# Kernel tuning notes

Hardware: AMD Instinct MI355X
Metric: run time of the kernel (lower is better)

## Reference

```python
import jax, jax.numpy as jnp
import numpy as np

N_NODES = 100000
FEAT = 128
N_EDGES = 1600000


def setup_inputs() -> dict:
    key = jax.random.key(0)
    k1, k2, k3, k4, k5 = jax.random.split(key, 5)
    weight = jax.random.normal(k1, (N_NODES, FEAT), dtype=jnp.float32)
    cj = jax.random.uniform(k2, (N_NODES, 1), dtype=jnp.float32)
    ci = jax.random.uniform(k3, (N_NODES, 1), dtype=jnp.float32)
    src = jax.random.randint(k4, (N_EDGES,), 0, N_NODES, dtype=jnp.int32)
    dst = jax.random.randint(k5, (N_EDGES,), 0, N_NODES, dtype=jnp.int32)
    return {"weight": weight, "cj": cj, "ci": ci, "src": src, "dst": dst}


def reference(weight, cj, ci, src, dst):
    # feat = weight * dropout(cj); dropout_rate=0.0 -> identity
    feat = weight * cj                      # [N, F]
    msgs = feat[src]                        # [E, F] copy_src gather
    h = jax.ops.segment_sum(msgs, dst, num_segments=weight.shape[0])  # [N, F]
    return h * ci                           # dst-side normalize
```

## Files before the change

kernel.cpp:

```cpp
#include <hip/hip_runtime.h>
#include <hip/hip_bf16.h>

#define FEAT 128
#define BINW 128
#define BINSHIFT 7
#define TB 8192
#define MAXBIN 1024
#define MAXTILE 256
#define FS_CAP 4096

__device__ __forceinline__ unsigned short f2b(float f) {
    __hip_bfloat16 h = __float2bfloat16(f);
    return *reinterpret_cast<unsigned short*>(&h);
}
__device__ __forceinline__ float b2f_lo(unsigned u) {
    unsigned x = u << 16;
    float f;
    __builtin_memcpy(&f, &x, 4);
    return f;
}
__device__ __forceinline__ float b2f_hi(unsigned u) {
    unsigned x = u & 0xFFFF0000u;
    float f;
    __builtin_memcpy(&f, &x, 4);
    return f;
}
__device__ __forceinline__ unsigned int pack2(float lo, float hi) {
    return (unsigned int)f2b(lo) | ((unsigned int)f2b(hi) << 16);
}


__global__ void convert_kernel(const float* __restrict__ weight,
                               const float* __restrict__ cj,
                               unsigned short* __restrict__ feat16, int N) {
    int i = blockIdx.x * 256 + threadIdx.x;
    if (i >= N * (FEAT / 8)) return;
    int row = i >> 4;
    int seg = i & 15;
    float c = cj[row];
    const float4* p = reinterpret_cast<const float4*>(weight + (size_t)row * FEAT + seg * 8);
    float4 a = p[0], b = p[1];
    uint4 o;
    o.x = pack2(a.x * c, a.y * c);
    o.y = pack2(a.z * c, a.w * c);
    o.z = pack2(b.x * c, b.y * c);
    o.w = pack2(b.z * c, b.w * c);
    *reinterpret_cast<uint4*>(feat16 + (size_t)i * 8) = o;
}

__global__ void hist_bins_kernel(const int* __restrict__ dst, int* __restrict__ cnt,
                                 int E, int NBIN) {
    __shared__ int h[MAXBIN];
    int tile = blockIdx.x;
    for (int b = threadIdx.x; b < NBIN; b += 256) h[b] = 0;
    __syncthreads();
    int e0 = tile * TB;
    #pragma unroll 4
    for (int i = 0; i < TB / 256; ++i) {
        int e = e0 + i * 256 + threadIdx.x;
        if (e < E) atomicAdd(&h[dst[e] >> BINSHIFT], 1);
    }
    __syncthreads();
    for (int b = threadIdx.x; b < NBIN; b += 256) cnt[tile * NBIN + b] = h[b];
}

__global__ void bin_scan_kernel(const int* __restrict__ cnt, int* __restrict__ base_local,
                                int* __restrict__ binTot, int NBIN, int NTILE) {
    __shared__ int s[MAXTILE];
    int b = blockIdx.x;
    int t = threadIdx.x;
    int v = (t < NTILE) ? cnt[(size_t)t * NBIN + b] : 0;
    s[t] = v;
    __syncthreads();
    for (int off = 1; off < MAXTILE; off <<= 1) {
        int u = (t >= off) ? s[t - off] : 0;
        __syncthreads();
        s[t] += u;
        __syncthreads();
    }
    if (t < NTILE) base_local[(size_t)t * NBIN + b] = s[t] - v;
    if (t == MAXTILE - 1) binTot[b] = s[t];
}

__global__ void scan_tot_kernel(const int* __restrict__ binTot, int* __restrict__ binStart,
                                int NBIN) {
    __shared__ int s[1024];
    int t = threadIdx.x;
    int v = (t < NBIN) ? binTot[t] : 0;
    s[t] = v;
    __syncthreads();
    for (int off = 1; off < 1024; off <<= 1) {
        int u = (t >= off) ? s[t - off] : 0;
        __syncthreads();
        s[t] += u;
        __syncthreads();
    }
    if (t < NBIN) binStart[t] = s[t] - v;
    if (t == NBIN - 1) binStart[NBIN] = s[t];
}

__global__ void scatter_pairs_kernel(const int* __restrict__ src, const int* __restrict__ dst,
                                     const int* __restrict__ base_local,
                                     const int* __restrict__ binStart,
                                     unsigned* __restrict__ pair,
                                     int E, int NBIN) {
    __shared__ int base_l[MAXBIN];
    __shared__ int cur[MAXBIN];
    int tile = blockIdx.x;
    for (int b = threadIdx.x; b < NBIN; b += 256) {
        base_l[b] = binStart[b] + base_local[(size_t)tile * NBIN + b];
        cur[b] = 0;
    }
    __syncthreads();
    int e0 = tile * TB;
    #pragma unroll 4
    for (int i = 0; i < TB / 256; ++i) {
        int e = e0 + i * 256 + threadIdx.x;
        if (e < E) {
            int d = dst[e];
            int b = d >> BINSHIFT;
            int pos = atomicAdd(&cur[b], 1);
            pair[base_l[b] + pos] = (unsigned)src[e] | ((unsigned)(d & (BINW - 1)) << 17);
        }
    }
}

__global__ void fine_sort_kernel(unsigned* __restrict__ pair,
                                 unsigned* __restrict__ tmp,
                                 const int* __restrict__ binStart,
                                 int* __restrict__ offsets,
                                 int N, int E) {
    __shared__ int cnt[BINW];
    __shared__ int sbase[BINW];
    __shared__ unsigned stage[FS_CAP];
    int bin = blockIdx.x;
    int t = threadIdx.x;
    if (t < BINW) cnt[t] = 0;
    __syncthreads();
    int start = binStart[bin];
    int end   = binStart[bin + 1];
    bool lds_ok = (end - start) <= FS_CAP;

    if (lds_ok) {
        for (int k = start + t; k < end; k += 256) {
            unsigned p = pair[k];
            stage[k - start] = p;
            atomicAdd(&cnt[p >> 17], 1);
        }
    } else {
        for (int k = start + t; k < end; k += 256) {
            unsigned p = pair[k];
            tmp[k] = p;
            atomicAdd(&cnt[p >> 17], 1);
        }
    }
    __syncthreads();
    int mine = (t < BINW) ? cnt[t] : 0;
    if (t < BINW) sbase[t] = mine;
    __syncthreads();
    for (int d = 1; d < BINW; d <<= 1) {
        int v = 0;
        if (t < BINW && t >= d) v = sbase[t - d];
        __syncthreads();
        if (t < BINW) sbase[t] += v;
        __syncthreads();
    }
    if (t < BINW) {
        int excl = sbase[t] - mine;
        int node = (bin << BINSHIFT) + t;
        if (node < N) offsets[node] = start + excl;
        sbase[t] = start + excl;
        cnt[t] = 0;
    }
    if (bin == 0 && t == 0) offsets[N] = E;
    __syncthreads();
    if (lds_ok) {
        for (int k = start + t; k < end; k += 256) {
            unsigned p = stage[k - start];
            int ld = p >> 17;
            int pos = atomicAdd(&cnt[ld], 1);
            pair[sbase[ld] + pos] = p & 0x1FFFF;
        }
    } else {
        for (int k = start + t; k < end; k += 256) {
            unsigned p = tmp[k];
            int ld = p >> 17;
            int pos = atomicAdd(&cnt[ld], 1);
            pair[sbase[ld] + pos] = p & 0x1FFFF;
        }
    }
}

__global__ void gather_kernel(const unsigned short* __restrict__ feat16,
                              const float* __restrict__ ci,
                              const int* __restrict__ offsets,
                              const int* __restrict__ src_sorted,
                              float* __restrict__ out, int N) {
    int gt = blockIdx.x * blockDim.x + threadIdx.x;
    int node = gt >> 6;
    if (node >= N) return;
    int lane = gt & 63;
    int fi   = (lane & 15) << 3;
    int q    = lane >> 4;
    int start = offsets[node];
    int end   = offsets[node + 1];
    float acc[8] = {0.f, 0.f, 0.f, 0.f, 0.f, 0.f, 0.f, 0.f};
    #pragma unroll 2
    for (int k = start + q; k < end; k += 4) {
        int s = src_sorted[k];
        uint4 u = *reinterpret_cast<const uint4*>(feat16 + ((size_t)s << 7) + fi);
        acc[0] += b2f_lo(u.x); acc[1] += b2f_hi(u.x);
        acc[2] += b2f_lo(u.y); acc[3] += b2f_hi(u.y);
        acc[4] += b2f_lo(u.z); acc[5] += b2f_hi(u.z);
        acc[6] += b2f_lo(u.w); acc[7] += b2f_hi(u.w);
    }
    #pragma unroll
    for (int j = 0; j < 8; ++j) {
        acc[j] += __shfl_xor(acc[j], 16);
        acc[j] += __shfl_xor(acc[j], 32);
    }
    if (q == 0) {
        float c = ci[node];
        float4 v0 = make_float4(acc[0] * c, acc[1] * c, acc[2] * c, acc[3] * c);
        float4 v1 = make_float4(acc[4] * c, acc[5] * c, acc[6] * c, acc[7] * c);
        float* o = out + ((size_t)node << 7) + fi;
        *reinterpret_cast<float4*>(o)     = v0;
        *reinterpret_cast<float4*>(o + 4) = v1;
    }
}


__global__ void zero_ints_kernel(int* __restrict__ p, int n) {
    int i = blockIdx.x * blockDim.x + threadIdx.x;
    if (i < n) p[i] = 0;
}

__global__ void convert_hist_kernel(const float* __restrict__ weight,
                                    const float* __restrict__ cj,
                                    const int* __restrict__ dst,
                                    int* __restrict__ counts,
                                    unsigned short* __restrict__ feat16,
                                    int N, int E) {
    int i = blockIdx.x * blockDim.x + threadIdx.x;
    int NC = N * (FEAT / 8);
    if (i < NC) {
        int row = i >> 4;
        int seg = i & 15;
        float c = cj[row];
        const float4* p = reinterpret_cast<const float4*>(weight + (size_t)row * FEAT + seg * 8);
        float4 a = p[0], b = p[1];
        uint4 o;
        o.x = pack2(a.x * c, a.y * c);
        o.y = pack2(a.z * c, a.w * c);
        o.z = pack2(b.x * c, b.y * c);
        o.w = pack2(b.z * c, b.w * c);
        *reinterpret_cast<uint4*>(feat16 + (size_t)i * 8) = o;
    }
    if (i < E) atomicAdd(&counts[dst[i]], 1);
}

__global__ void block_sum_kernel(const int* __restrict__ counts, int* __restrict__ bsum, int N) {
    __shared__ int s[256];
    int i = blockIdx.x * 256 + threadIdx.x;
    s[threadIdx.x] = (i < N) ? counts[i] : 0;
    __syncthreads();
    for (int off = 128; off > 0; off >>= 1) {
        if (threadIdx.x < off) s[threadIdx.x] += s[threadIdx.x + off];
        __syncthreads();
    }
    if (threadIdx.x == 0) bsum[blockIdx.x] = s[0];
}

__global__ void scan_bsum_kernel(int* __restrict__ bsum, int nb) {
    __shared__ int s[512];
    int t = threadIdx.x;
    int mine = (t < nb) ? bsum[t] : 0;
    s[t] = mine;
    __syncthreads();
    for (int off = 1; off < 512; off <<= 1) {
        int v = (t >= off) ? s[t - off] : 0;
        __syncthreads();
        s[t] += v;
        __syncthreads();
    }
    if (t < nb) bsum[t] = s[t] - mine;
}

__global__ void scan_counts_kernel(const int* __restrict__ counts, const int* __restrict__ bsum,
                                   int* __restrict__ offsets, int* __restrict__ cursor,
                                   int N, int E) {
    __shared__ int s[256];
    int t = threadIdx.x;
    int i = blockIdx.x * 256 + t;
    int mine = (i < N) ? counts[i] : 0;
    s[t] = mine;
    __syncthreads();
    for (int off = 1; off < 256; off <<= 1) {
        int v = (t >= off) ? s[t - off] : 0;
        __syncthreads();
        s[t] += v;
        __syncthreads();
    }
    if (i < N) {
        int o = bsum[blockIdx.x] + s[t] - mine;
        offsets[i] = o;
        cursor[i] = o;
    }
    if (i == 0 && blockIdx.x == 0) offsets[N] = E;
}

__global__ void bucket_kernel(const int* __restrict__ src, const int* __restrict__ dst,
                              int* __restrict__ cursor,
                              int* __restrict__ src_sorted, int E) {
    int i = blockIdx.x * blockDim.x + threadIdx.x;
    if (i < E) {
        int pos = atomicAdd(&cursor[dst[i]], 1);
        src_sorted[pos] = src[i];
    }
}


__global__ void gcmc_zero_kernel(float4* __restrict__ out, int n4) {
    int i = blockIdx.x * blockDim.x + threadIdx.x;
    if (i < n4) out[i] = make_float4(0.f, 0.f, 0.f, 0.f);
}

__global__ void gcmc_scatter_kernel(const float* __restrict__ weight,
                                    const float* __restrict__ cj,
                                    const int* __restrict__ src,
                                    const int* __restrict__ dst,
                                    float* __restrict__ out,
                                    int n_edges) {
    int t = blockIdx.x * blockDim.x + threadIdx.x;
    int e = t >> 5;
    int f = (t & 31) << 2;
    if (e >= n_edges) return;
    int s = src[e];
    int d = dst[e];
    float c = cj[s];
    const float4 w = *reinterpret_cast<const float4*>(weight + (size_t)s * FEAT + f);
    float* o = out + (size_t)d * FEAT + f;
    unsafeAtomicAdd(o + 0, w.x * c);
    unsafeAtomicAdd(o + 1, w.y * c);
    unsafeAtomicAdd(o + 2, w.z * c);
    unsafeAtomicAdd(o + 3, w.w * c);
}

__global__ void gcmc_scale_kernel(float4* __restrict__ out,
                                  const float* __restrict__ ci, int n4) {
    int i = blockIdx.x * blockDim.x + threadIdx.x;
    if (i < n4) {
        float c = ci[i >> 5];
        float4 v = out[i];
        v.x *= c; v.y *= c; v.z *= c; v.w *= c;
        out[i] = v;
    }
}


static inline size_t align256(size_t x) { return (x + 255) & ~(size_t)255; }

extern "C" void kernel_launch(void* const* d_in, const int* in_sizes, int n_in,
                              void* d_out, int out_size, void* d_ws, size_t ws_size,
                              hipStream_t stream) {
    const float* weight = (const float*)d_in[0];
    const float* cj     = (const float*)d_in[1];
    const float* ci     = (const float*)d_in[2];
    const int*   src    = (const int*)d_in[3];
    const int*   dst    = (const int*)d_in[4];
    float* out = (float*)d_out;

    const int N = in_sizes[1];
    const int E = in_sizes[3];

    const int NBIN  = (N + BINW - 1) >> BINSHIFT;
    const int NTILE = (E + TB - 1) / TB;

    size_t o_feat = 0;
    size_t o_pair = align256(o_feat + (size_t)N * FEAT * 2);
    size_t o_cnt  = align256(o_pair + (size_t)E * 4);
    size_t o_base = align256(o_cnt + (size_t)NTILE * NBIN * 4);
    size_t o_tot  = align256(o_base + (size_t)NTILE * NBIN * 4);
    size_t o_bs   = align256(o_tot + (size_t)NBIN * 4);
    size_t o_off  = align256(o_bs + (size_t)(NBIN + 1) * 4);
    size_t need_new = o_off + (size_t)(N + 1) * 4;

    if (ws_size >= need_new && NBIN <= MAXBIN && NTILE <= MAXTILE &&
        N <= (1 << 17) && out_size >= E) {
        char* ws = (char*)d_ws;
        unsigned short* feat16 = (unsigned short*)(ws + o_feat);
        unsigned* pair   = (unsigned*)(ws + o_pair);
        int* cnt         = (int*)(ws + o_cnt);
        int* base_local  = (int*)(ws + o_base);
        int* binTot      = (int*)(ws + o_tot);
        int* binStart    = (int*)(ws + o_bs);
        int* offsets     = (int*)(ws + o_off);

        convert_kernel<<<(N * (FEAT / 8) + 255) / 256, 256, 0, stream>>>(
            weight, cj, feat16, N);
        hist_bins_kernel<<<NTILE, 256, 0, stream>>>(dst, cnt, E, NBIN);
        bin_scan_kernel<<<NBIN, MAXTILE, 0, stream>>>(cnt, base_local, binTot, NBIN, NTILE);
        scan_tot_kernel<<<1, 1024, 0, stream>>>(binTot, binStart, NBIN);
        scatter_pairs_kernel<<<NTILE, 256, 0, stream>>>(src, dst, base_local, binStart,
                                                        pair, E, NBIN);
        fine_sort_kernel<<<NBIN, 256, 0, stream>>>(pair, (unsigned*)out, binStart,
                                                   offsets, N, E);
        long threads = (long)N * 64;
        gather_kernel<<<(int)((threads + 255) / 256), 256, 0, stream>>>(
            feat16, ci, offsets, (const int*)pair, out, N);
        return;
    }

    const int NB = (N + 255) / 256;
    size_t m_off = 0;
    size_t m_cur = align256(m_off + (size_t)(N + 1) * 4);
    size_t m_bsm = align256(m_cur + (size_t)N * 4);
    size_t m_src = align256(m_bsm + 512 * 4);
    size_t m_ft  = align256(m_src + (size_t)E * 4);
    size_t need_mid = m_ft + (size_t)N * FEAT * 2;

    if (ws_size >= need_mid && NB <= 512) {
        char* ws = (char*)d_ws;
        int* offsets    = (int*)(ws + m_off);
        int* cursor     = (int*)(ws + m_cur);
        int* bsum       = (int*)(ws + m_bsm);
        int* src_sorted = (int*)(ws + m_src);
        unsigned short* feat16 = (unsigned short*)(ws + m_ft);

        zero_ints_kernel<<<NB, 256, 0, stream>>>(cursor, N);
        {
            long T = (long)N * (FEAT / 8);
            if ((long)E > T) T = E;
            convert_hist_kernel<<<(int)((T + 255) / 256), 256, 0, stream>>>(
                weight, cj, dst, cursor, feat16, N, E);
        }
        block_sum_kernel<<<NB, 256, 0, stream>>>(cursor, bsum, N);
        scan_bsum_kernel<<<1, 512, 0, stream>>>(bsum, NB);
        scan_counts_kernel<<<NB, 256, 0, stream>>>(cursor, bsum, offsets, cursor, N, E);
        bucket_kernel<<<(E + 255) / 256, 256, 0, stream>>>(src, dst, cursor, src_sorted, E);
        long threads = (long)N * 64;
        gather_kernel<<<(int)((threads + 255) / 256), 256, 0, stream>>>(
            feat16, ci, offsets, src_sorted, out, N);
        return;
    }

    const int total = N * FEAT;
    const int n4 = total >> 2;
    gcmc_zero_kernel<<<(n4 + 255) / 256, 256, 0, stream>>>((float4*)out, n4);
    const long threads = (long)E * 32;
    gcmc_scatter_kernel<<<(int)((threads + 255) / 256), 256, 0, stream>>>(
        weight, cj, src, dst, out, E);
    gcmc_scale_kernel<<<(n4 + 255) / 256, 256, 0, stream>>>((float4*)out, ci, n4);
}
```

Before: 132.1 us.

## Fuse convert into histogram kernel, shrink edge tiles, unroll gather more

Merges the bf16 feature conversion into the destination-bin histogram kernel so both run in one launch, splitting the conversion work across the histogram tiles. Edge tile size drops from 8192 to 2048 (chosen at runtime), which raises the tile count to about 782 and gives the histogram and scatter kernels more blocks. MAXTILE grows to 1024 to match, so the per-bin scan now runs 1024-thread blocks. The gather loop unroll goes from 2 to 4. The costs are larger count arrays, a heavier scan, and more blocks each doing a small amount of work.

```diff
diff --git a/kernel.cpp b/kernel.cpp
--- a/kernel.cpp
+++ b/kernel.cpp
@@ -4,9 +4,8 @@
 #define FEAT 128
 #define BINW 128
 #define BINSHIFT 7
-#define TB 8192
 #define MAXBIN 1024
-#define MAXTILE 256
+#define MAXTILE 1024
 #define FS_CAP 4096
 
 __device__ __forceinline__ unsigned short f2b(float f) {
@@ -30,38 +29,45 @@
 }
 
 
-__global__ void convert_kernel(const float* __restrict__ weight,
-                               const float* __restrict__ cj,
-                               unsigned short* __restrict__ feat16, int N) {
-    int i = blockIdx.x * 256 + threadIdx.x;
-    if (i >= N * (FEAT / 8)) return;
-    int row = i >> 4;
-    int seg = i & 15;
-    float c = cj[row];
-    const float4* p = reinterpret_cast<const float4*>(weight + (size_t)row * FEAT + seg * 8);
-    float4 a = p[0], b = p[1];
-    uint4 o;
-    o.x = pack2(a.x * c, a.y * c);
-    o.y = pack2(a.z * c, a.w * c);
-    o.z = pack2(b.x * c, b.y * c);
-    o.w = pack2(b.z * c, b.w * c);
-    *reinterpret_cast<uint4*>(feat16 + (size_t)i * 8) = o;
-}
-
-__global__ void hist_bins_kernel(const int* __restrict__ dst, int* __restrict__ cnt,
-                                 int E, int NBIN) {
+__global__ void convert_hist_bins_kernel(const float* __restrict__ weight,
+                                         const float* __restrict__ cj,
+                                         const int* __restrict__ dst,
+                                         unsigned short* __restrict__ feat16,
+                                         int* __restrict__ cnt,
+                                         int N, int E, int NBIN, int tb, int ipt) {
     __shared__ int h[MAXBIN];
     int tile = blockIdx.x;
     for (int b = threadIdx.x; b < NBIN; b += 256) h[b] = 0;
     __syncthreads();
-    int e0 = tile * TB;
-    #pragma unroll 4
-    for (int i = 0; i < TB / 256; ++i) {
+
+    int NC = N * (FEAT / 8);
+    int cbase = tile * 256 * ipt;
+    for (int j = 0; j < ipt; ++j) {
+        int i = cbase + j * 256 + threadIdx.x;
+        if (i < NC) {
+            int row = i >> 4;
+            int seg = i & 15;
+            float c = cj[row];
+            const float4* p = reinterpret_cast<const float4*>(
+                weight + (size_t)row * FEAT + seg * 8);
+            float4 a = p[0], b4 = p[1];
+            uint4 o;
+            o.x = pack2(a.x * c, a.y * c);
+            o.y = pack2(a.z * c, a.w * c);
+            o.z = pack2(b4.x * c, b4.y * c);
+            o.w = pack2(b4.z * c, b4.w * c);
+            *reinterpret_cast<uint4*>(feat16 + (size_t)i * 8) = o;
+        }
+    }
+
+    int e0 = tile * tb;
+    int iters = tb >> 8;
+    for (int i = 0; i < iters; ++i) {
         int e = e0 + i * 256 + threadIdx.x;
         if (e < E) atomicAdd(&h[dst[e] >> BINSHIFT], 1);
     }
     __syncthreads();
-    for (int b = threadIdx.x; b < NBIN; b += 256) cnt[tile * NBIN + b] = h[b];
+    for (int b = threadIdx.x; b < NBIN; b += 256) cnt[(size_t)tile * NBIN + b] = h[b];
 }
 
 __global__ void bin_scan_kernel(const int* __restrict__ cnt, int* __restrict__ base_local,
@@ -103,7 +109,7 @@
                                      const int* __restrict__ base_local,
                                      const int* __restrict__ binStart,
                                      unsigned* __restrict__ pair,
-                                     int E, int NBIN) {
+                                     int E, int NBIN, int tb) {
     __shared__ int base_l[MAXBIN];
     __shared__ int cur[MAXBIN];
     int tile = blockIdx.x;
@@ -112,9 +118,9 @@
         cur[b] = 0;
     }
     __syncthreads();
-    int e0 = tile * TB;
-    #pragma unroll 4
-    for (int i = 0; i < TB / 256; ++i) {
+    int e0 = tile * tb;
+    int iters = tb >> 8;
+    for (int i = 0; i < iters; ++i) {
         int e = e0 + i * 256 + threadIdx.x;
         if (e < E) {
             int d = dst[e];
@@ -205,7 +211,7 @@
     int start = offsets[node];
     int end   = offsets[node + 1];
     float acc[8] = {0.f, 0.f, 0.f, 0.f, 0.f, 0.f, 0.f, 0.f};
-    #pragma unroll 2
+    #pragma unroll 4
     for (int k = start + q; k < end; k += 4) {
         int s = src_sorted[k];
         uint4 u = *reinterpret_cast<const uint4*>(feat16 + ((size_t)s << 7) + fi);
@@ -373,20 +379,23 @@
     const int N = in_sizes[1];
     const int E = in_sizes[3];
 
-    const int NBIN  = (N + BINW - 1) >> BINSHIFT;
-    const int NTILE = (E + TB - 1) / TB;
-
-    size_t o_feat = 0;
-    size_t o_pair = align256(o_feat + (size_t)N * FEAT * 2);
-    size_t o_cnt  = align256(o_pair + (size_t)E * 4);
-    size_t o_base = align256(o_cnt + (size_t)NTILE * NBIN * 4);
-    size_t o_tot  = align256(o_base + (size_t)NTILE * NBIN * 4);
-    size_t o_bs   = align256(o_tot + (size_t)NBIN * 4);
-    size_t o_off  = align256(o_bs + (size_t)(NBIN + 1) * 4);
-    size_t need_new = o_off + (size_t)(N + 1) * 4;
-
-    if (ws_size >= need_new && NBIN <= MAXBIN && NTILE <= MAXTILE &&
-        N <= (1 << 17) && out_size >= E) {
+    const int NBIN = (N + BINW - 1) >> BINSHIFT;
+
+    for (int tb = 2048; tb <= 8192; tb *= 4) {
+        const int NTILE = (E + tb - 1) / tb;
+        if (NTILE > MAXTILE) continue;
+
+        size_t o_feat = 0;
+        size_t o_pair = align256(o_feat + (size_t)N * FEAT * 2);
+        size_t o_cnt  = align256(o_pair + (size_t)E * 4);
+        size_t o_base = align256(o_cnt + (size_t)NTILE * NBIN * 4);
+        size_t o_tot  = align256(o_base + (size_t)NTILE * NBIN * 4);
+        size_t o_bs   = align256(o_tot + (size_t)NBIN * 4);
+        size_t o_off  = align256(o_bs + (size_t)(NBIN + 1) * 4);
+        size_t need   = o_off + (size_t)(N + 1) * 4;
+
+        if (ws_size < need || NBIN > MAXBIN || N > (1 << 17) || out_size < E) continue;
+
         char* ws = (char*)d_ws;
         unsigned short* feat16 = (unsigned short*)(ws + o_feat);
         unsigned* pair   = (unsigned*)(ws + o_pair);
@@ -396,13 +405,15 @@
         int* binStart    = (int*)(ws + o_bs);
         int* offsets     = (int*)(ws + o_off);
 
-        convert_kernel<<<(N * (FEAT / 8) + 255) / 256, 256, 0, stream>>>(
-            weight, cj, feat16, N);
-        hist_bins_kernel<<<NTILE, 256, 0, stream>>>(dst, cnt, E, NBIN);
+        const int NC  = N * (FEAT / 8);
+        const int ipt = (NC + NTILE * 256 - 1) / (NTILE * 256);
+
+        convert_hist_bins_kernel<<<NTILE, 256, 0, stream>>>(
+            weight, cj, dst, feat16, cnt, N, E, NBIN, tb, ipt);
         bin_scan_kernel<<<NBIN, MAXTILE, 0, stream>>>(cnt, base_local, binTot, NBIN, NTILE);
         scan_tot_kernel<<<1, 1024, 0, stream>>>(binTot, binStart, NBIN);
         scatter_pairs_kernel<<<NTILE, 256, 0, stream>>>(src, dst, base_local, binStart,
-                                                        pair, E, NBIN);
+                                                        pair, E, NBIN, tb);
         fine_sort_kernel<<<NBIN, 256, 0, stream>>>(pair, (unsigned*)out, binStart,
                                                    offsets, N, E);
         long threads = (long)N * 64;
```

Result: no change. 131.4 us (-0.5%).
